# Performance work log

Hardware: AMD Instinct MI355X
Metric: run time of the kernel (lower is better)

The kernel has to match this reference:

```python
import jax, jax.numpy as jnp
import numpy as np

E, H, W = 1024, 16, 256  # embed_dim, num_heads, window_size
D = E // H               # head_dim


def _rmsnorm(t, w):
    eps = jnp.finfo(t.dtype).eps
    return t * jax.lax.rsqrt(jnp.mean(t * t, axis=-1, keepdims=True) + eps) * w


def setup_inputs() -> dict:
    key = jax.random.key(0)
    ks = jax.random.split(key, 11)
    B, T = 2, 2048
    s = 1.0 / np.sqrt(E)
    return {
        "x": jax.random.normal(ks[0], (B, T, E), jnp.float32),
        "wq": jax.random.normal(ks[1], (E, E), jnp.float32) * s,
        "bq": jnp.zeros((E,), jnp.float32),
        "wk": jax.random.normal(ks[2], (E, E), jnp.float32) * s,
        "bk": jnp.zeros((E,), jnp.float32),
        "wv": jax.random.normal(ks[3], (E, E), jnp.float32) * s,
        "bv": jnp.zeros((E,), jnp.float32),
        "wo": jax.random.normal(ks[4], (E, E), jnp.float32) * s,
        "bo": jnp.zeros((E,), jnp.float32),
        "qn_w": jnp.ones((D,), jnp.float32),
        "kn_w": jnp.ones((D,), jnp.float32),
    }


def reference(x, wq, bq, wk, bk, wv, bv, wo, bo, qn_w, kn_w):
    B, T, _ = x.shape
    # projections; weights stored (in, out)
    q = (x @ wq + bq).reshape(B, T, H, D).transpose(0, 2, 1, 3)  # [B,H,T,D]
    k = (x @ wk + bk).reshape(B, T, H, D).transpose(0, 2, 1, 3)
    v = (x @ wv + bv).reshape(B, T, H, D).transpose(0, 2, 1, 3)
    q = _rmsnorm(q, qn_w)
    k = _rmsnorm(k, kn_w)

    scores = jnp.einsum("bhqd,bhkd->bhqk", q, k) / jnp.sqrt(jnp.float32(D))
    row = jnp.arange(T)[:, None]
    col = jnp.arange(T)[None, :]
    invalid = (col > row) | (row - col >= W)  # causal + sliding window
    neg_inf = jnp.float32(-jnp.inf)
    scores = jnp.where(invalid, neg_inf, scores)

    # genetic fitness reweighting
    masked_attn = jnp.where(invalid, 0.0, jax.nn.softmax(scores, axis=-1))
    gene_means = jnp.mean(jax.nn.sigmoid(masked_attn), axis=-1)  # [B,H,T]
    denom = gene_means + 0.5
    sum_inv = jnp.sum(1.0 / denom, axis=2, keepdims=True)        # [B,H,1]
    fitness = 1.0 / (denom * sum_inv)                            # [B,H,T]
    scores = scores + jnp.log(fitness)[..., None]

    attn = jax.nn.softmax(scores, axis=-1)
    out = jnp.einsum("bhqk,bhkd->bhqd", attn, v)
    out = out.transpose(0, 2, 1, 3).reshape(B, T, E)
    return out @ wo + bo
```

## Files before the change

kernel.cpp:

```cpp
#include <hip/hip_runtime.h>

typedef _Float16 f16;
typedef _Float16 f16x4 __attribute__((ext_vector_type(4)));
typedef _Float16 f16x8 __attribute__((ext_vector_type(8)));
typedef float f32x4 __attribute__((ext_vector_type(4)));

#define MFMA16(a, b, c) __builtin_amdgcn_mfma_f32_16x16x32_f16(a, b, c, 0, 0, 0)

constexpr int T = 2048;
constexpr int E = 1024;
constexpr int H = 16;
constexpr int D = 64;
constexpr int WIN = 256;
#define NEGF (-1e30f)
#define L2E 1.4426950408889634f

__device__ __forceinline__ void gload16(const f16* g, f16* l) {
  __builtin_amdgcn_global_load_lds(
      (__attribute__((address_space(1))) void*)(void*)g,
      (__attribute__((address_space(3))) void*)(void*)l, 16, 0, 0);
}

__global__ __launch_bounds__(256) void cast_x_kernel(const float* __restrict__ x,
                                                     f16* __restrict__ xb) {
  int idx = (blockIdx.x * 256 + threadIdx.x) * 4;
  float4 v = *(const float4*)(x + idx);
  f16x4 o = {(f16)v.x, (f16)v.y, (f16)v.z, (f16)v.w};
  *(f16x4*)(xb + idx) = o;
}

__global__ __launch_bounds__(256) void transpose_w_kernel(
    const float* __restrict__ w0, const float* __restrict__ w1,
    const float* __restrict__ w2, const float* __restrict__ w3,
    f16* __restrict__ o0, f16* __restrict__ o1, f16* __restrict__ o2,
    f16* __restrict__ o3) {
  int z = blockIdx.z;
  const float* w = z == 0 ? w0 : z == 1 ? w1 : z == 2 ? w2 : w3;
  f16* o = z == 0 ? o0 : z == 1 ? o1 : z == 2 ? o2 : o3;
  __shared__ float tile[64][65];
  int k0 = blockIdx.x * 64, n0 = blockIdx.y * 64;
  int r = threadIdx.x >> 2, cb = (threadIdx.x & 3) * 16;
  const float* src = w + (size_t)(k0 + r) * E + n0 + cb;
#pragma unroll
  for (int j = 0; j < 16; j += 4) {
    float4 v = *(const float4*)(src + j);
    tile[r][cb + j] = v.x;
    tile[r][cb + j + 1] = v.y;
    tile[r][cb + j + 2] = v.z;
    tile[r][cb + j + 3] = v.w;
  }
  __syncthreads();
  f16 tmp[16];
#pragma unroll
  for (int j = 0; j < 16; ++j) tmp[j] = (f16)tile[cb + j][r];
  f16* dst = o + (size_t)(n0 + r) * E + k0 + cb;
  *(f16x8*)dst = *(f16x8*)&tmp[0];
  *(f16x8*)(dst + 8) = *(f16x8*)&tmp[8];
}

__global__ __launch_bounds__(256) void qkv_fused_kernel(
    const f16* __restrict__ A, const f16* __restrict__ Bq,
    const f16* __restrict__ Bk, const f16* __restrict__ Bv,
    const float* __restrict__ cq, const float* __restrict__ ck,
    const float* __restrict__ cv, const float* __restrict__ qnw,
    const float* __restrict__ knw, f16* __restrict__ oq, f16* __restrict__ ok,
    f16* __restrict__ Vt) {
  const int K = E, N = E;
  __shared__ f16 lA[2][8192];
  __shared__ f16 lB[3][2][8192];

  int m0 = blockIdx.x * 128, n0 = blockIdx.y * 128;
  int tid = threadIdx.x;
  int wid = tid >> 6, lane = tid & 63;
  int wm = wid >> 1, wn = wid & 1;
  int lr = lane & 15, lg = lane >> 4;

  f32x4 zero = {0.f, 0.f, 0.f, 0.f};
  f32x4 acc[3][4][4];
#pragma unroll
  for (int z = 0; z < 3; ++z)
    for (int a = 0; a < 4; ++a)
      for (int b = 0; b < 4; ++b) acc[z][a][b] = zero;

  int srow = lane >> 3;
  int scol = (lane & 7) << 3;

  auto stage = [&](int buf, int k0) {
#pragma unroll
    for (int p = 0; p < 4; ++p) {
      int cc = (wid << 2) + p;
      int row = (cc << 3) + srow;
      int gc = scol ^ ((row & 7) << 3);
      size_t ga = (size_t)(m0 + row) * K + k0 + gc;
      size_t gb = (size_t)(n0 + row) * K + k0 + gc;
      gload16(A + ga, &lA[buf][cc << 9]);
      gload16(Bq + gb, &lB[0][buf][cc << 9]);
      gload16(Bk + gb, &lB[1][buf][cc << 9]);
      gload16(Bv + gb, &lB[2][buf][cc << 9]);
    }
  };

  stage(0, 0);
  __syncthreads();
  int cur = 0;
  for (int t = 0; t < 16; ++t) {
    if (t + 1 < 16) stage(cur ^ 1, (t + 1) << 6);
#pragma unroll
    for (int kk = 0; kk < 2; ++kk) {
      int kc = kk * 32 + (lg << 3);
      f16x8 af[4];
#pragma unroll
      for (int mt = 0; mt < 4; ++mt) {
        int row = wm * 64 + mt * 16 + lr;
        af[mt] = *(const f16x8*)&lA[cur][((row << 6) + kc) ^ ((row & 7) << 3)];
      }
#pragma unroll
      for (int z = 0; z < 3; ++z) {
#pragma unroll
        for (int nt = 0; nt < 4; ++nt) {
          int row = wn * 64 + nt * 16 + lr;
          f16x8 bf =
              *(const f16x8*)&lB[z][cur][((row << 6) + kc) ^ ((row & 7) << 3)];
#pragma unroll
          for (int mt = 0; mt < 4; ++mt)
            acc[z][mt][nt] = MFMA16(af[mt], bf, acc[z][mt][nt]);
        }
      }
    }
    if (t + 1 < 16) {
      __syncthreads();
      cur ^= 1;
    }
  }

  const float eps = 1.1920929e-7f;
#pragma unroll
  for (int z = 0; z < 2; ++z) {
    const float* nw = z == 0 ? qnw : knw;
    const float* bias = z == 0 ? cq : ck;
    f16* o = z == 0 ? oq : ok;
    const float osc = z == 0 ? 0.125f : 1.0f;
    float wv_[4];
#pragma unroll
    for (int nt = 0; nt < 4; ++nt) wv_[nt] = nw[nt * 16 + lr] * osc;
#pragma unroll
    for (int mt = 0; mt < 4; ++mt) {
      float vbuf[4][4];
      float ss[4] = {0.f, 0.f, 0.f, 0.f};
#pragma unroll
      for (int nt = 0; nt < 4; ++nt) {
        float bv = bias[n0 + wn * 64 + nt * 16 + lr];
#pragma unroll
        for (int i = 0; i < 4; ++i) {
          float v = acc[z][mt][nt][i] + bv;
          vbuf[nt][i] = v;
          ss[i] += v * v;
        }
      }
      float rr[4];
#pragma unroll
      for (int i = 0; i < 4; ++i) {
        ss[i] += __shfl_xor(ss[i], 1);
        ss[i] += __shfl_xor(ss[i], 2);
        ss[i] += __shfl_xor(ss[i], 4);
        ss[i] += __shfl_xor(ss[i], 8);
        rr[i] = rsqrtf(ss[i] * (1.0f / 64.0f) + eps);
      }
      int row = m0 + wm * 64 + mt * 16 + (lg << 2);
#pragma unroll
      for (int nt = 0; nt < 4; ++nt) {
        int col = n0 + wn * 64 + nt * 16 + lr;
#pragma unroll
        for (int i = 0; i < 4; ++i)
          o[(size_t)(row + i) * N + col] = (f16)(vbuf[nt][i] * rr[i] * wv_[nt]);
      }
    }
  }
#pragma unroll
  for (int mt = 0; mt < 4; ++mt) {
    int row = m0 + wm * 64 + mt * 16 + (lg << 2);
    int b = row >> 11;
    int t = row & (T - 1);
#pragma unroll
    for (int nt = 0; nt < 4; ++nt) {
      int col = n0 + wn * 64 + nt * 16 + lr;
      float bv = cv[col];
      int h = col >> 6, d = col & 63;
      f16x4 pk = {(f16)(acc[2][mt][nt][0] + bv), (f16)(acc[2][mt][nt][1] + bv),
                  (f16)(acc[2][mt][nt][2] + bv), (f16)(acc[2][mt][nt][3] + bv)};
      *(f16x4*)&Vt[(((size_t)(b * H + h) * D + d) << 11) + t] = pk;
    }
  }
}

__global__ __launch_bounds__(256) void out_gemm_kernel(
    const f16* __restrict__ A, const f16* __restrict__ Bt,
    const float* __restrict__ bias, float* __restrict__ out, int M, int N,
    int K) {
  __shared__ f16 lA[2][8192];
  __shared__ f16 lB[2][8192];

  int m0 = blockIdx.x * 128, n0 = blockIdx.y * 128;
  int tid = threadIdx.x;
  int wid = tid >> 6, lane = tid & 63;
  int wm = wid >> 1, wn = wid & 1;
  int lr = lane & 15, lg = lane >> 4;

  f32x4 zero = {0.f, 0.f, 0.f, 0.f};
  f32x4 acc[4][4];
  for (int a = 0; a < 4; ++a)
    for (int b = 0; b < 4; ++b) acc[a][b] = zero;

  int srow = lane >> 3;
  int scol = (lane & 7) << 3;

  auto stage = [&](int buf, int k0) {
#pragma unroll
    for (int p = 0; p < 4; ++p) {
      int cc = (wid << 2) + p;
      int row = (cc << 3) + srow;
      int gc = scol ^ ((row & 7) << 3);
      gload16(A + (size_t)(m0 + row) * K + k0 + gc, &lA[buf][cc << 9]);
      gload16(Bt + (size_t)(n0 + row) * K + k0 + gc, &lB[buf][cc << 9]);
    }
  };

  int nit = K >> 6;
  stage(0, 0);
  __syncthreads();
  int cur = 0;
  for (int t = 0; t < nit; ++t) {
    if (t + 1 < nit) stage(cur ^ 1, (t + 1) << 6);
#pragma unroll
    for (int kk = 0; kk < 2; ++kk) {
      int kc = kk * 32 + (lg << 3);
      f16x8 af[4], bf[4];
#pragma unroll
      for (int mt = 0; mt < 4; ++mt) {
        int row = wm * 64 + mt * 16 + lr;
        af[mt] = *(const f16x8*)&lA[cur][((row << 6) + kc) ^ ((row & 7) << 3)];
      }
#pragma unroll
      for (int nt = 0; nt < 4; ++nt) {
        int row = wn * 64 + nt * 16 + lr;
        bf[nt] = *(const f16x8*)&lB[cur][((row << 6) + kc) ^ ((row & 7) << 3)];
      }
#pragma unroll
      for (int mt = 0; mt < 4; ++mt)
#pragma unroll
        for (int nt = 0; nt < 4; ++nt)
          acc[mt][nt] = MFMA16(af[mt], bf[nt], acc[mt][nt]);
    }
    if (t + 1 < nit) {
      __syncthreads();
      cur ^= 1;
    }
  }

#pragma unroll
  for (int mt = 0; mt < 4; ++mt) {
#pragma unroll
    for (int nt = 0; nt < 4; ++nt) {
      int row = m0 + wm * 64 + mt * 16 + (lg << 2);
      int col = n0 + wn * 64 + nt * 16 + lr;
      float bv = bias[col];
#pragma unroll
      for (int i = 0; i < 4; ++i)
        out[(size_t)(row + i) * N + col] = acc[mt][nt][i] + bv;
    }
  }
}

__global__ __launch_bounds__(256) void attn_kernel(const f16* __restrict__ qn,
                                                   const f16* __restrict__ kn,
                                                   const f16* __restrict__ Vt,
                                                   f16* __restrict__ aout) {
  int q0 = blockIdx.x * 64;
  int bh = blockIdx.y;
  int b = bh >> 4, h = bh & 15;
  int tid = threadIdx.x;
  int w = tid >> 6, lane = tid & 63;
  int lr = lane & 15, lg = lane >> 4;

  __shared__ f16 lK[2][4096];
  __shared__ f16 lV[2][4096];
  __shared__ f16 lP[4096];

  const f16* Qb = qn + (size_t)(b * T + q0 + w * 16 + lr) * E + h * 64 + (lg << 3);
  f16x8 qf0 = *(const f16x8*)Qb;
  f16x8 qf1 = *(const f16x8*)(Qb + 32);

  f32x4 zero = {0.f, 0.f, 0.f, 0.f};
  f32x4 acc[4] = {zero, zero, zero, zero};
  float m[4] = {NEGF, NEGF, NEGF, NEGF};
  float l[4] = {0.f, 0.f, 0.f, 0.f};

  int mi = q0 >> 6;
  int kts = mi - 4 < 0 ? 0 : mi - 4;

  const f16* Kbase = kn + (size_t)b * T * E + h * 64;
  const f16* Vbase = Vt + (size_t)bh * D * T;

  int srow = lane >> 3;
  int scol = (lane & 7) << 3;

  auto stageKV = [&](int buf, int kt) {
    int k0 = kt << 6;
#pragma unroll
    for (int p = 0; p < 2; ++p) {
      int cc = (w << 1) + p;
      int row = (cc << 3) + srow;
      int gc = scol ^ ((row & 7) << 3);
      gload16(Kbase + (size_t)(k0 + row) * E + gc, &lK[buf][cc << 9]);
      gload16(Vbase + (size_t)row * T + k0 + gc, &lV[buf][cc << 9]);
    }
  };

  stageKV(0, kts);
  __syncthreads();
  int cur = 0;

  for (int kt = kts; kt <= mi; ++kt) {
    if (kt < mi) stageKV(cur ^ 1, kt + 1);
    int k0 = kt << 6;

    f32x4 s[4];
#pragma unroll
    for (int ct = 0; ct < 4; ++ct) s[ct] = zero;
#pragma unroll
    for (int kk = 0; kk < 2; ++kk) {
      int kc = kk * 32 + (lg << 3);
#pragma unroll
      for (int ct = 0; ct < 4; ++ct) {
        int row = ct * 16 + lr;
        f16x8 bf = *(const f16x8*)&lK[cur][((row << 6) + kc) ^ ((row & 7) << 3)];
        s[ct] = MFMA16(kk == 0 ? qf0 : qf1, bf, s[ct]);
      }
    }

    float tm[4] = {NEGF, NEGF, NEGF, NEGF};
    int rowg0 = q0 + w * 16 + (lg << 2);
    bool needmask = (kt == mi) || (mi >= 4 && kt == kts);
    if (needmask) {
#pragma unroll
      for (int ct = 0; ct < 4; ++ct) {
        int col = k0 + ct * 16 + lr;
#pragma unroll
        for (int i = 0; i < 4; ++i) {
          int rowg = rowg0 + i;
          float v = s[ct][i];
          if (col > rowg || rowg - col >= WIN) v = NEGF;
          s[ct][i] = v;
          tm[i] = fmaxf(tm[i], v);
        }
      }
    } else {
#pragma unroll
      for (int ct = 0; ct < 4; ++ct)
#pragma unroll
        for (int i = 0; i < 4; ++i) tm[i] = fmaxf(tm[i], s[ct][i]);
    }
#pragma unroll
    for (int i = 0; i < 4; ++i) {
      tm[i] = fmaxf(tm[i], __shfl_xor(tm[i], 1));
      tm[i] = fmaxf(tm[i], __shfl_xor(tm[i], 2));
      tm[i] = fmaxf(tm[i], __shfl_xor(tm[i], 4));
      tm[i] = fmaxf(tm[i], __shfl_xor(tm[i], 8));
    }
    bool up = (tm[0] > m[0]) || (tm[1] > m[1]) || (tm[2] > m[2]) ||
              (tm[3] > m[3]);
    if (__any(up)) {
      float fac[4];
#pragma unroll
      for (int i = 0; i < 4; ++i) {
        float mn = fmaxf(m[i], tm[i]);
        fac[i] = exp2f((m[i] - mn) * L2E);
        m[i] = mn;
        l[i] *= fac[i];
      }
#pragma unroll
      for (int dt = 0; dt < 4; ++dt)
#pragma unroll
        for (int i = 0; i < 4; ++i) acc[dt][i] *= fac[i];
    }
    float ps[4] = {0.f, 0.f, 0.f, 0.f};
#pragma unroll
    for (int ct = 0; ct < 4; ++ct)
#pragma unroll
      for (int i = 0; i < 4; ++i) {
        float p = exp2f((s[ct][i] - m[i]) * L2E);
        s[ct][i] = p;
        ps[i] += p;
      }
#pragma unroll
    for (int i = 0; i < 4; ++i) {
      ps[i] += __shfl_xor(ps[i], 1);
      ps[i] += __shfl_xor(ps[i], 2);
      ps[i] += __shfl_xor(ps[i], 4);
      ps[i] += __shfl_xor(ps[i], 8);
      l[i] += ps[i];
    }

#pragma unroll
    for (int ct = 0; ct < 4; ++ct)
#pragma unroll
      for (int i = 0; i < 4; ++i) {
        int qloc = (lg << 2) + i;
        int el = (qloc << 6) + ct * 16 + lr;
        lP[w * 1024 + (el ^ ((qloc & 7) << 3))] = (f16)s[ct][i];
      }

#pragma unroll
    for (int kk = 0; kk < 2; ++kk) {
      int kc = kk * 32 + (lg << 3);
      int ep = w * 1024 + (((lr << 6) + kc) ^ ((lr & 7) << 3));
      f16x8 pf = *(const f16x8*)&lP[ep];
#pragma unroll
      for (int dt = 0; dt < 4; ++dt) {
        int row = dt * 16 + lr;
        f16x8 vf = *(const f16x8*)&lV[cur][((row << 6) + kc) ^ ((row & 7) << 3)];
        acc[dt] = MFMA16(pf, vf, acc[dt]);
      }
    }

    if (kt < mi) {
      __syncthreads();
      cur ^= 1;
    }
  }

#pragma unroll
  for (int i = 0; i < 4; ++i) {
    float inv = 1.0f / l[i];
    int tok = q0 + w * 16 + (lg << 2) + i;
    f16* dst = aout + (size_t)(b * T + tok) * E + h * 64 + lr;
#pragma unroll
    for (int dt = 0; dt < 4; ++dt) dst[dt * 16] = (f16)(acc[dt][i] * inv);
  }
}

extern "C" void kernel_launch(void* const* d_in, const int* in_sizes, int n_in,
                              void* d_out, int out_size, void* d_ws,
                              size_t ws_size, hipStream_t stream) {
  const float* x = (const float*)d_in[0];
  const float* wq = (const float*)d_in[1];
  const float* bq = (const float*)d_in[2];
  const float* wk = (const float*)d_in[3];
  const float* bk = (const float*)d_in[4];
  const float* wv = (const float*)d_in[5];
  const float* bv = (const float*)d_in[6];
  const float* wo = (const float*)d_in[7];
  const float* bo = (const float*)d_in[8];
  const float* qn_w = (const float*)d_in[9];
  const float* kn_w = (const float*)d_in[10];
  float* out = (float*)d_out;

  char* ws = (char*)d_ws;
  const size_t MB = 1u << 20;
  f16* xb = (f16*)(ws);
  f16* wqT = (f16*)(ws + 8 * MB);
  f16* wkT = (f16*)(ws + 10 * MB);
  f16* wvT = (f16*)(ws + 12 * MB);
  f16* woT = (f16*)(ws + 14 * MB);
  f16* qn = (f16*)(ws + 16 * MB);
  f16* kn = (f16*)(ws + 24 * MB);
  f16* Vt = (f16*)(ws + 32 * MB);
  f16* aout = (f16*)(ws + 40 * MB);

  cast_x_kernel<<<4096, 256, 0, stream>>>(x, xb);
  transpose_w_kernel<<<dim3(16, 16, 4), 256, 0, stream>>>(wq, wk, wv, wo, wqT,
                                                          wkT, wvT, woT);
  qkv_fused_kernel<<<dim3(32, 8), 256, 0, stream>>>(
      xb, wqT, wkT, wvT, bq, bk, bv, qn_w, kn_w, qn, kn, Vt);
  attn_kernel<<<dim3(32, 32), 256, 0, stream>>>(qn, kn, Vt, aout);
  out_gemm_kernel<<<dim3(32, 8), 256, 0, stream>>>(aout, woT, bo, out, 4096,
                                                   1024, 1024);
}
```

Baseline: 107.7 us.

## Split QKV GEMM per projection, shrink out-GEMM tiles, merge prep kernels, swizzle blocks

Merges the x cast and weight transpose into a single prep launch. The fused QKV GEMM is split so each projection runs in its own z-slice, giving 768 blocks instead of 256 with less LDS and fewer accumulators per block. The output GEMM tile shrinks to 128x64 for 512 blocks, and all GEMM and attention grids use a block-index swizzle meant to improve L2 locality. The split QKV reloads the A tile three times, trading extra global traffic for higher occupancy and more parallelism on the many-CU GPU.

```diff
diff --git a/kernel.cpp b/kernel.cpp
--- a/kernel.cpp
+++ b/kernel.cpp
@@ -21,24 +21,25 @@
       (__attribute__((address_space(3))) void*)(void*)l, 16, 0, 0);
 }
 
-__global__ __launch_bounds__(256) void cast_x_kernel(const float* __restrict__ x,
-                                                     f16* __restrict__ xb) {
-  int idx = (blockIdx.x * 256 + threadIdx.x) * 4;
-  float4 v = *(const float4*)(x + idx);
-  f16x4 o = {(f16)v.x, (f16)v.y, (f16)v.z, (f16)v.w};
-  *(f16x4*)(xb + idx) = o;
-}
-
-__global__ __launch_bounds__(256) void transpose_w_kernel(
+__global__ __launch_bounds__(256) void prep_kernel(
+    const float* __restrict__ x, f16* __restrict__ xb,
     const float* __restrict__ w0, const float* __restrict__ w1,
     const float* __restrict__ w2, const float* __restrict__ w3,
     f16* __restrict__ o0, f16* __restrict__ o1, f16* __restrict__ o2,
     f16* __restrict__ o3) {
-  int z = blockIdx.z;
+  if (blockIdx.x < 4096) {
+    int idx = (blockIdx.x * 256 + threadIdx.x) * 4;
+    float4 v = *(const float4*)(x + idx);
+    f16x4 o = {(f16)v.x, (f16)v.y, (f16)v.z, (f16)v.w};
+    *(f16x4*)(xb + idx) = o;
+    return;
+  }
+  int bid = blockIdx.x - 4096;
+  int z = bid >> 8;
   const float* w = z == 0 ? w0 : z == 1 ? w1 : z == 2 ? w2 : w3;
   f16* o = z == 0 ? o0 : z == 1 ? o1 : z == 2 ? o2 : o3;
   __shared__ float tile[64][65];
-  int k0 = blockIdx.x * 64, n0 = blockIdx.y * 64;
+  int k0 = ((bid >> 4) & 15) * 64, n0 = (bid & 15) * 64;
   int r = threadIdx.x >> 2, cb = (threadIdx.x & 3) * 16;
   const float* src = w + (size_t)(k0 + r) * E + n0 + cb;
 #pragma unroll
@@ -58,29 +59,33 @@
   *(f16x8*)(dst + 8) = *(f16x8*)&tmp[8];
 }
 
-__global__ __launch_bounds__(256) void qkv_fused_kernel(
-    const f16* __restrict__ A, const f16* __restrict__ Bq,
-    const f16* __restrict__ Bk, const f16* __restrict__ Bv,
-    const float* __restrict__ cq, const float* __restrict__ ck,
-    const float* __restrict__ cv, const float* __restrict__ qnw,
+__global__ __launch_bounds__(256) void qkv_gemm_kernel(
+    const f16* __restrict__ A, const f16* __restrict__ B0,
+    const f16* __restrict__ B1, const f16* __restrict__ B2,
+    const float* __restrict__ c0, const float* __restrict__ c1,
+    const float* __restrict__ c2, const float* __restrict__ qnw,
     const float* __restrict__ knw, f16* __restrict__ oq, f16* __restrict__ ok,
     f16* __restrict__ Vt) {
   const int K = E, N = E;
+  int z = blockIdx.z;
+  const f16* Bt = z == 0 ? B0 : z == 1 ? B1 : B2;
+  const float* bias = z == 0 ? c0 : z == 1 ? c1 : c2;
+
   __shared__ f16 lA[2][8192];
-  __shared__ f16 lB[3][2][8192];
-
-  int m0 = blockIdx.x * 128, n0 = blockIdx.y * 128;
+  __shared__ f16 lB[2][8192];
+
+  int sw = ((blockIdx.x & 7) << 5) + (blockIdx.x >> 3);
+  int m0 = (sw >> 3) << 7, n0 = (sw & 7) << 7;
+
   int tid = threadIdx.x;
   int wid = tid >> 6, lane = tid & 63;
   int wm = wid >> 1, wn = wid & 1;
   int lr = lane & 15, lg = lane >> 4;
 
   f32x4 zero = {0.f, 0.f, 0.f, 0.f};
-  f32x4 acc[3][4][4];
-#pragma unroll
-  for (int z = 0; z < 3; ++z)
-    for (int a = 0; a < 4; ++a)
-      for (int b = 0; b < 4; ++b) acc[z][a][b] = zero;
+  f32x4 acc[4][4];
+  for (int a = 0; a < 4; ++a)
+    for (int b = 0; b < 4; ++b) acc[a][b] = zero;
 
   int srow = lane >> 3;
   int scol = (lane & 7) << 3;
@@ -91,12 +96,8 @@
       int cc = (wid << 2) + p;
       int row = (cc << 3) + srow;
       int gc = scol ^ ((row & 7) << 3);
-      size_t ga = (size_t)(m0 + row) * K + k0 + gc;
-      size_t gb = (size_t)(n0 + row) * K + k0 + gc;
-      gload16(A + ga, &lA[buf][cc << 9]);
-      gload16(Bq + gb, &lB[0][buf][cc << 9]);
-      gload16(Bk + gb, &lB[1][buf][cc << 9]);
-      gload16(Bv + gb, &lB[2][buf][cc << 9]);
+      gload16(A + (size_t)(m0 + row) * K + k0 + gc, &lA[buf][cc << 9]);
+      gload16(Bt + (size_t)(n0 + row) * K + k0 + gc, &lB[buf][cc << 9]);
     }
   };
 
@@ -108,24 +109,22 @@
 #pragma unroll
     for (int kk = 0; kk < 2; ++kk) {
       int kc = kk * 32 + (lg << 3);
-      f16x8 af[4];
+      f16x8 af[4], bf[4];
 #pragma unroll
       for (int mt = 0; mt < 4; ++mt) {
         int row = wm * 64 + mt * 16 + lr;
         af[mt] = *(const f16x8*)&lA[cur][((row << 6) + kc) ^ ((row & 7) << 3)];
       }
 #pragma unroll
-      for (int z = 0; z < 3; ++z) {
-#pragma unroll
-        for (int nt = 0; nt < 4; ++nt) {
-          int row = wn * 64 + nt * 16 + lr;
-          f16x8 bf =
-              *(const f16x8*)&lB[z][cur][((row << 6) + kc) ^ ((row & 7) << 3)];
-#pragma unroll
-          for (int mt = 0; mt < 4; ++mt)
-            acc[z][mt][nt] = MFMA16(af[mt], bf, acc[z][mt][nt]);
-        }
-      }
+      for (int nt = 0; nt < 4; ++nt) {
+        int row = wn * 64 + nt * 16 + lr;
+        bf[nt] = *(const f16x8*)&lB[cur][((row << 6) + kc) ^ ((row & 7) << 3)];
+      }
+#pragma unroll
+      for (int mt = 0; mt < 4; ++mt)
+#pragma unroll
+        for (int nt = 0; nt < 4; ++nt)
+          acc[mt][nt] = MFMA16(af[mt], bf[nt], acc[mt][nt]);
     }
     if (t + 1 < 16) {
       __syncthreads();
@@ -133,12 +132,10 @@
     }
   }
 
-  const float eps = 1.1920929e-7f;
-#pragma unroll
-  for (int z = 0; z < 2; ++z) {
+  if (z < 2) {
     const float* nw = z == 0 ? qnw : knw;
-    const float* bias = z == 0 ? cq : ck;
     f16* o = z == 0 ? oq : ok;
+    const float eps = 1.1920929e-7f;
     const float osc = z == 0 ? 0.125f : 1.0f;
     float wv_[4];
 #pragma unroll
@@ -152,7 +149,7 @@
         float bv = bias[n0 + wn * 64 + nt * 16 + lr];
 #pragma unroll
         for (int i = 0; i < 4; ++i) {
-          float v = acc[z][mt][nt][i] + bv;
+          float v = acc[mt][nt][i] + bv;
           vbuf[nt][i] = v;
           ss[i] += v * v;
         }
@@ -175,41 +172,44 @@
           o[(size_t)(row + i) * N + col] = (f16)(vbuf[nt][i] * rr[i] * wv_[nt]);
       }
     }
-  }
-#pragma unroll
-  for (int mt = 0; mt < 4; ++mt) {
-    int row = m0 + wm * 64 + mt * 16 + (lg << 2);
-    int b = row >> 11;
-    int t = row & (T - 1);
-#pragma unroll
-    for (int nt = 0; nt < 4; ++nt) {
-      int col = n0 + wn * 64 + nt * 16 + lr;
-      float bv = cv[col];
-      int h = col >> 6, d = col & 63;
-      f16x4 pk = {(f16)(acc[2][mt][nt][0] + bv), (f16)(acc[2][mt][nt][1] + bv),
-                  (f16)(acc[2][mt][nt][2] + bv), (f16)(acc[2][mt][nt][3] + bv)};
-      *(f16x4*)&Vt[(((size_t)(b * H + h) * D + d) << 11) + t] = pk;
+  } else {
+#pragma unroll
+    for (int mt = 0; mt < 4; ++mt) {
+      int row = m0 + wm * 64 + mt * 16 + (lg << 2);
+      int b = row >> 11;
+      int t = row & (T - 1);
+#pragma unroll
+      for (int nt = 0; nt < 4; ++nt) {
+        int col = n0 + wn * 64 + nt * 16 + lr;
+        float bv = bias[col];
+        int h = col >> 6, d = col & 63;
+        f16x4 pk = {(f16)(acc[mt][nt][0] + bv), (f16)(acc[mt][nt][1] + bv),
+                    (f16)(acc[mt][nt][2] + bv), (f16)(acc[mt][nt][3] + bv)};
+        *(f16x4*)&Vt[(((size_t)(b * H + h) * D + d) << 11) + t] = pk;
+      }
     }
   }
 }
 
 __global__ __launch_bounds__(256) void out_gemm_kernel(
     const f16* __restrict__ A, const f16* __restrict__ Bt,
-    const float* __restrict__ bias, float* __restrict__ out, int M, int N,
-    int K) {
+    const float* __restrict__ bias, float* __restrict__ out) {
+  const int K = E, N = E;
   __shared__ f16 lA[2][8192];
-  __shared__ f16 lB[2][8192];
-
-  int m0 = blockIdx.x * 128, n0 = blockIdx.y * 128;
+  __shared__ f16 lB[2][4096];
+
+  int sw = ((blockIdx.x & 7) << 6) + (blockIdx.x >> 3);
+  int m0 = (sw >> 4) << 7, n0 = (sw & 15) << 6;
+
   int tid = threadIdx.x;
   int wid = tid >> 6, lane = tid & 63;
   int wm = wid >> 1, wn = wid & 1;
   int lr = lane & 15, lg = lane >> 4;
 
   f32x4 zero = {0.f, 0.f, 0.f, 0.f};
-  f32x4 acc[4][4];
+  f32x4 acc[4][2];
   for (int a = 0; a < 4; ++a)
-    for (int b = 0; b < 4; ++b) acc[a][b] = zero;
+    for (int b = 0; b < 2; ++b) acc[a][b] = zero;
 
   int srow = lane >> 3;
   int scol = (lane & 7) << 3;
@@ -221,37 +221,42 @@
       int row = (cc << 3) + srow;
       int gc = scol ^ ((row & 7) << 3);
       gload16(A + (size_t)(m0 + row) * K + k0 + gc, &lA[buf][cc << 9]);
+    }
+#pragma unroll
+    for (int p = 0; p < 2; ++p) {
+      int cc = (wid << 1) + p;
+      int row = (cc << 3) + srow;
+      int gc = scol ^ ((row & 7) << 3);
       gload16(Bt + (size_t)(n0 + row) * K + k0 + gc, &lB[buf][cc << 9]);
     }
   };
 
-  int nit = K >> 6;
   stage(0, 0);
   __syncthreads();
   int cur = 0;
-  for (int t = 0; t < nit; ++t) {
-    if (t + 1 < nit) stage(cur ^ 1, (t + 1) << 6);
+  for (int t = 0; t < 16; ++t) {
+    if (t + 1 < 16) stage(cur ^ 1, (t + 1) << 6);
 #pragma unroll
     for (int kk = 0; kk < 2; ++kk) {
       int kc = kk * 32 + (lg << 3);
-      f16x8 af[4], bf[4];
+      f16x8 af[4], bf[2];
 #pragma unroll
       for (int mt = 0; mt < 4; ++mt) {
         int row = wm * 64 + mt * 16 + lr;
         af[mt] = *(const f16x8*)&lA[cur][((row << 6) + kc) ^ ((row & 7) << 3)];
       }
 #pragma unroll
-      for (int nt = 0; nt < 4; ++nt) {
-        int row = wn * 64 + nt * 16 + lr;
+      for (int nt = 0; nt < 2; ++nt) {
+        int row = wn * 32 + nt * 16 + lr;
         bf[nt] = *(const f16x8*)&lB[cur][((row << 6) + kc) ^ ((row & 7) << 3)];
       }
 #pragma unroll
       for (int mt = 0; mt < 4; ++mt)
 #pragma unroll
-        for (int nt = 0; nt < 4; ++nt)
+        for (int nt = 0; nt < 2; ++nt)
           acc[mt][nt] = MFMA16(af[mt], bf[nt], acc[mt][nt]);
     }
-    if (t + 1 < nit) {
+    if (t + 1 < 16) {
       __syncthreads();
       cur ^= 1;
     }
@@ -260,9 +265,9 @@
 #pragma unroll
   for (int mt = 0; mt < 4; ++mt) {
 #pragma unroll
-    for (int nt = 0; nt < 4; ++nt) {
+    for (int nt = 0; nt < 2; ++nt) {
       int row = m0 + wm * 64 + mt * 16 + (lg << 2);
-      int col = n0 + wn * 64 + nt * 16 + lr;
+      int col = n0 + wn * 32 + nt * 16 + lr;
       float bv = bias[col];
 #pragma unroll
       for (int i = 0; i < 4; ++i)
@@ -275,8 +280,9 @@
                                                    const f16* __restrict__ kn,
                                                    const f16* __restrict__ Vt,
                                                    f16* __restrict__ aout) {
-  int q0 = blockIdx.x * 64;
-  int bh = blockIdx.y;
+  int sw = ((blockIdx.x & 7) << 7) + (blockIdx.x >> 3);
+  int q0 = (sw & 31) << 6;
+  int bh = sw >> 5;
   int b = bh >> 4, h = bh & 15;
   int tid = threadIdx.x;
   int w = tid >> 6, lane = tid & 63;
@@ -467,12 +473,10 @@
   f16* Vt = (f16*)(ws + 32 * MB);
   f16* aout = (f16*)(ws + 40 * MB);
 
-  cast_x_kernel<<<4096, 256, 0, stream>>>(x, xb);
-  transpose_w_kernel<<<dim3(16, 16, 4), 256, 0, stream>>>(wq, wk, wv, wo, wqT,
-                                                          wkT, wvT, woT);
-  qkv_fused_kernel<<<dim3(32, 8), 256, 0, stream>>>(
+  prep_kernel<<<5120, 256, 0, stream>>>(x, xb, wq, wk, wv, wo, wqT, wkT, wvT,
+                                        woT);
+  qkv_gemm_kernel<<<dim3(256, 1, 3), 256, 0, stream>>>(
       xb, wqT, wkT, wvT, bq, bk, bv, qn_w, kn_w, qn, kn, Vt);
-  attn_kernel<<<dim3(32, 32), 256, 0, stream>>>(qn, kn, Vt, aout);
-  out_gemm_kernel<<<dim3(32, 8), 256, 0, stream>>>(aout, woT, bo, out, 4096,
-                                                   1024, 1024);
-}
+  attn_kernel<<<1024, 256, 0, stream>>>(qn, kn, Vt, aout);
+  out_gemm_kernel<<<512, 256, 0, stream>>>(aout, woT, bo, out);
+}
```

Measured after the change: 107.2 us. About the same (-0.5%).
